# Optimization experiments

Hardware: AMD Instinct MI355X
Metric: run time of the kernel (lower is better)

The kernel has to match this reference:

```python
import jax, jax.numpy as jnp
import numpy as np
import math

B, S, E, D = 8, 2048, 1024, 1024  # batch, seq, emb_dim, encoder_emb_dim
LN_EPS = 1e-5
CLAMP = 1.0e9

def setup_inputs() -> dict:
    key = jax.random.key(0)
    ks = jax.random.split(key, 6)
    s = 1.0 / math.sqrt(E)
    return {
        "x": jax.random.normal(ks[0], (B, S, E), dtype=jnp.float32),
        "ln_w": jnp.ones((E,), jnp.float32),
        "ln_b": jnp.zeros((E,), jnp.float32),
        "wq": jax.random.normal(ks[1], (E, D), jnp.float32) * s,
        "bq": jnp.zeros((D,), jnp.float32),
        "wk": jax.random.normal(ks[2], (E, D), jnp.float32) * s,
        "bk": jnp.zeros((D,), jnp.float32),
        "wv": jax.random.normal(ks[3], (E, D), jnp.float32) * s,
        "bv": jnp.zeros((D,), jnp.float32),
        "w0": jax.random.normal(ks[4], (D, E), jnp.float32) * (1.0 / math.sqrt(D)),
        "b0": jnp.zeros((E,), jnp.float32),
    }

def reference(x, ln_w, ln_b, wq, bq, wk, bk, wv, bv, w0, b0):
    # LayerNorm over last dim (torch default eps=1e-5)
    mu = jnp.mean(x, axis=-1, keepdims=True)
    var = jnp.mean(jnp.square(x - mu), axis=-1, keepdims=True)
    xn = (x - mu) * jax.lax.rsqrt(var + LN_EPS) * ln_w + ln_b

    q = xn @ wq + bq  # [B,S,D]
    k = xn @ wk + bk
    v = xn @ wv + bv

    scale = math.sqrt(D) + 1e-9
    scores = jnp.einsum("bsd,btd->bst", q, k) / scale
    scores = jnp.clip(scores, -CLAMP, CLAMP)

    # masking=True, self_attending=True: mask = tril(ones, diagonal=-1)
    # i.e. positions t < s get -inf; diagonal stays unmasked (no NaN rows).
    mask = jnp.tril(jnp.ones((S, S), dtype=bool), k=-1)
    scores = jnp.where(mask, -jnp.inf, scores)

    a = jax.nn.softmax(scores, axis=-1)
    h = jnp.einsum("bst,btd->bsd", a, v)
    return h @ w0 + b0
```

## Files before the change

kernel.cpp:

```cpp
#include <hip/hip_runtime.h>
#include <cmath>

using u16 = unsigned short;
using u32 = unsigned int;
using bf16x8 = __attribute__((ext_vector_type(8))) __bf16;
using f32x4  = __attribute__((ext_vector_type(4))) float;

__device__ inline u16 f2bf(float f) {
  u32 u = __float_as_uint(f);
  u32 r = (u + 0x7fffu + ((u >> 16) & 1u)) >> 16;
  return (u16)r;
}
__device__ inline float bf2f(u16 v) { return __uint_as_float(((u32)v) << 16); }

__global__ __launch_bounds__(256) void prep1(
    const float* __restrict__ x, const float* __restrict__ lnw,
    const float* __restrict__ lnb, const float* __restrict__ wq,
    const float* __restrict__ wk, const float* __restrict__ wv,
    const float* __restrict__ w0, const float* __restrict__ bq,
    const float* __restrict__ bk, const float* __restrict__ bv,
    u16* __restrict__ xn, u16* __restrict__ w0t, u16* __restrict__ wqb,
    u16* __restrict__ wkb, u16* __restrict__ wvb, float* __restrict__ uvec,
    float* __restrict__ vvec, float* __restrict__ wb, float* __restrict__ sb) {
  int b = blockIdx.x;
  int tid = threadIdx.x;
  __shared__ float red[4];
  __shared__ float red2[4];
  int lane = tid & 63, wave = tid >> 6;
  if (b < 16384) {
    const float4* xr = (const float4*)(x + (size_t)b * 1024);
    float4 v = xr[tid];
    float s  = v.x + v.y + v.z + v.w;
    float ss = v.x * v.x + v.y * v.y + v.z * v.z + v.w * v.w;
#pragma unroll
    for (int o = 32; o >= 1; o >>= 1) {
      s  += __shfl_xor(s, o, 64);
      ss += __shfl_xor(ss, o, 64);
    }
    if (lane == 0) { red[wave] = s; red2[wave] = ss; }
    __syncthreads();
    s  = red[0] + red[1] + red[2] + red[3];
    ss = red2[0] + red2[1] + red2[2] + red2[3];
    float mean = s * (1.0f / 1024.0f);
    float var  = ss * (1.0f / 1024.0f) - mean * mean;
    float rstd = rsqrtf(var + 1e-5f);
    int c = tid * 4;
    ushort4 ov;
    ov.x = f2bf((v.x - mean) * rstd * lnw[c + 0] + lnb[c + 0]);
    ov.y = f2bf((v.y - mean) * rstd * lnw[c + 1] + lnb[c + 1]);
    ov.z = f2bf((v.z - mean) * rstd * lnw[c + 2] + lnb[c + 2]);
    ov.w = f2bf((v.w - mean) * rstd * lnw[c + 3] + lnb[c + 3]);
    ((ushort4*)(xn + (size_t)b * 1024))[tid] = ov;
  } else if (b < 17408) {
    int b2 = b - 16384;
    int c0 = (b2 & 31) * 32, r0 = (b2 >> 5) * 32;
    int tx = tid & 31, ty = tid >> 5;
    __shared__ float tile[32][33];
#pragma unroll
    for (int i = 0; i < 32; i += 8)
      tile[ty + i][tx] = w0[(size_t)(r0 + ty + i) * 1024 + c0 + tx];
    __syncthreads();
#pragma unroll
    for (int i = 0; i < 32; i += 8)
      w0t[(size_t)(c0 + ty + i) * 1024 + r0 + tx] = f2bf(tile[tx][ty + i]);
  } else if (b < 18944) {
    int b3 = b - 17408;
    int mat = b3 / 512, blk = b3 % 512;
    const float* src = (mat == 0) ? wq : (mat == 1) ? wk : wv;
    u16* dst = (mat == 0) ? wqb : (mat == 1) ? wkb : wvb;
    size_t base = (size_t)blk * 2048 + (size_t)tid * 8;
#pragma unroll
    for (int i = 0; i < 8; ++i) dst[base + i] = f2bf(src[base + i]);
  } else if (b < 22016) {
    int b4 = b - 18944;
    int which = b4 >> 10, idx = b4 & 1023;
    float p = 0.f;
    if (which == 0) {
      const float* r = wq + (size_t)idx * 1024;
      for (int e = tid * 4; e < (tid + 1) * 4; ++e) p += r[e] * bk[e];
    } else if (which == 1) {
      const float* r = wk + (size_t)idx * 1024;
      for (int e = tid * 4; e < (tid + 1) * 4; ++e) p += r[e] * bq[e];
    } else {
      for (int d = tid * 4; d < (tid + 1) * 4; ++d)
        p += bv[d] * w0[(size_t)d * 1024 + idx];
    }
#pragma unroll
    for (int o = 32; o >= 1; o >>= 1) p += __shfl_xor(p, o, 64);
    if (lane == 0) red[wave] = p;
    __syncthreads();
    if (tid == 0) {
      float t = red[0] + red[1] + red[2] + red[3];
      if (which == 0) uvec[idx] = t;
      else if (which == 1) vvec[idx] = t;
      else wb[idx] = t;
    }
  } else {
    float p = 0.f;
    for (int e = tid * 4; e < (tid + 1) * 4; ++e) p += bq[e] * bk[e];
#pragma unroll
    for (int o = 32; o >= 1; o >>= 1) p += __shfl_xor(p, o, 64);
    if (lane == 0) red[wave] = p;
    __syncthreads();
    if (tid == 0) sb[0] = red[0] + red[1] + red[2] + red[3];
  }
}

template <int OUTF32, int MODE>
__global__ __launch_bounds__(512, 2) void gemm256(
    const u16* __restrict__ A, const u16* __restrict__ B, void* __restrict__ Cv,
    const float* __restrict__ bias, int K, int lda, int ldb, int ldc,
    float scale, long long sA, long long sB, long long sC) {
  int gx = gridDim.x;
  int wg = blockIdx.y * gx + blockIdx.x;
  {
    int nwg = gx * gridDim.y;
    if ((nwg & 7) == 0) {
      int q = nwg >> 3;
      wg = (wg & 7) * q + (wg >> 3);
    }
  }
  const int ti = wg / gx, tj = wg % gx, bz = blockIdx.z;
  if (MODE == 1 && tj < ti) return;

  const u16* Ab = A + (size_t)bz * (size_t)sA;
  const u16* Bb = B + (size_t)bz * (size_t)sB;

  __shared__ u16 As[2][256 * 64];
  __shared__ u16 Bs[2][256 * 64];

  const int tid = threadIdx.x;
  const int wave = tid >> 6, lane = tid & 63;
  const int wr = wave >> 2, wc = wave & 3;
  const int fr = lane & 15;
  const int kb16 = (lane >> 4) * 16;
  const int swz = (fr & 7) << 4;
  const int cs0 = kb16 ^ swz;
  const int cs1 = (64 + kb16) ^ swz;
  const int aRowOff = (wr * 128 + fr) * 128;
  const int bRowOff = (wc * 64 + fr) * 128;

  size_t gAo[2][2], gBo[2][2];
  u32 ldsA[2][2], ldsB[2][2];
#pragma unroll
  for (int h = 0; h < 2; ++h) {
#pragma unroll
    for (int l = 0; l < 2; ++l) {
      int i = l * 512 + tid;
      int rih = i >> 3, ch8 = i & 7;
      int rA = (rih & 63) + ((rih >> 6) << 7) + h * 64;
      int cbA = (ch8 << 4) ^ ((rA & 7) << 4);
      gAo[h][l] = (size_t)rA * lda + (cbA >> 1);
      ldsA[h][l] = (u32)(rA * 8 + ch8) * 16;
      int rB = (rih & 31) + ((rih >> 5) << 6) + h * 32;
      int cbB = (ch8 << 4) ^ ((rB & 7) << 4);
      gBo[h][l] = (size_t)rB * ldb + (cbB >> 1);
      ldsB[h][l] = (u32)(rB * 8 + ch8) * 16;
    }
  }
  const size_t aBase = (size_t)(ti * 256) * lda;
  const size_t bBase = (size_t)(tj * 256) * ldb;

  const int k0 = (MODE == 2) ? ti * 256 : 0;
  const int niter = (K - k0) / 128;

  f32x4 acc[8][4] = {};
  bf16x8 aF[4][2], bF[4][2];

#define GLL(gaddr, laddr)                                        \
  __builtin_amdgcn_global_load_lds(                              \
      (const __attribute__((address_space(1))) void*)(gaddr),    \
      (__attribute__((address_space(3))) void*)(laddr), 16, 0, 0)

#define STAGE_A(buf, h, t)                                                     \
  do {                                                                         \
    const size_t _kt = aBase + (size_t)(k0 + (t) * 64);                        \
    GLL(Ab + _kt + gAo[h][0], (char*)&As[buf][0] + ldsA[h][0]);                \
    GLL(Ab + _kt + gAo[h][1], (char*)&As[buf][0] + ldsA[h][1]);                \
  } while (0)
#define STAGE_B(buf, h, t)                                                     \
  do {                                                                         \
    const size_t _kt = bBase + (size_t)(k0 + (t) * 64);                        \
    GLL(Bb + _kt + gBo[h][0], (char*)&Bs[buf][0] + ldsB[h][0]);                \
    GLL(Bb + _kt + gBo[h][1], (char*)&Bs[buf][0] + ldsB[h][1]);                \
  } while (0)

#define DS_A(buf, qm)                                                \
  do {                                                               \
    const char* _pa = (const char*)&As[buf][0] + aRowOff + (qm)*8192;\
    _Pragma("unroll") for (int mm = 0; mm < 4; ++mm) {               \
      aF[mm][0] = *(const bf16x8*)(_pa + mm * 2048 + cs0);           \
      aF[mm][1] = *(const bf16x8*)(_pa + mm * 2048 + cs1);           \
    }                                                                \
  } while (0)
#define DS_B(buf, nh)                                                \
  do {                                                               \
    const char* _pb = (const char*)&Bs[buf][0] + bRowOff;            \
    _Pragma("unroll") for (int nn = 0; nn < 2; ++nn) {               \
      bF[(nh)*2 + nn][0] = *(const bf16x8*)(_pb + ((nh)*2 + nn) * 2048 + cs0); \
      bF[(nh)*2 + nn][1] = *(const bf16x8*)(_pb + ((nh)*2 + nn) * 2048 + cs1); \
    }                                                                \
  } while (0)

#define MMA(qm, nh)                                                          \
  do {                                                                       \
    _Pragma("unroll") for (int mm = 0; mm < 4; ++mm)                         \
    _Pragma("unroll") for (int nn = 0; nn < 2; ++nn) {                       \
      f32x4 _c = acc[(qm)*4 + mm][(nh)*2 + nn];                              \
      _c = __builtin_amdgcn_mfma_f32_16x16x32_bf16(aF[mm][0], bF[(nh)*2+nn][0], _c, 0, 0, 0); \
      _c = __builtin_amdgcn_mfma_f32_16x16x32_bf16(aF[mm][1], bF[(nh)*2+nn][1], _c, 0, 0, 0); \
      acc[(qm)*4 + mm][(nh)*2 + nn] = _c;                                    \
    }                                                                        \
  } while (0)

#define BAR __builtin_amdgcn_s_barrier()
#define LGKM0 asm volatile("s_waitcnt lgkmcnt(0)" ::: "memory")
#define VM6 asm volatile("s_waitcnt vmcnt(6)" ::: "memory")
#define VM0 asm volatile("s_waitcnt vmcnt(0)" ::: "memory")
#define PRIO1 __builtin_amdgcn_s_setprio(1)
#define PRIO0 __builtin_amdgcn_s_setprio(0)

  STAGE_B(0, 0, 0); STAGE_B(0, 1, 0); STAGE_A(0, 0, 0); STAGE_A(0, 1, 0);
  STAGE_B(1, 0, 1); STAGE_B(1, 1, 1); STAGE_A(1, 0, 1);
  VM6; BAR;

  for (int it = 0; it < niter; ++it) {
    const bool last = (it == niter - 1);
    const int t1g = 2 * it + 1, t2g = 2 * it + 2, t3g = 2 * it + 3;

    DS_A(0, 0); DS_B(0, 0);
    STAGE_A(1, 1, t1g);
    BAR; LGKM0; PRIO1; MMA(0, 0); PRIO0; BAR;
    DS_B(0, 1);
    if (!last) STAGE_B(0, 0, t2g);
    BAR; LGKM0; PRIO1; MMA(0, 1); PRIO0; BAR;
    DS_A(0, 1);
    if (!last) STAGE_B(0, 1, t2g);
    BAR; LGKM0; PRIO1; MMA(1, 0); PRIO0; BAR;
    if (!last) STAGE_A(0, 0, t2g);
    BAR; PRIO1; MMA(1, 1); PRIO0;
    if (last) { VM0; } else { VM6; }
    BAR;
    DS_A(1, 0); DS_B(1, 0);
    if (!last) STAGE_A(0, 1, t2g);
    BAR; LGKM0; PRIO1; MMA(0, 0); PRIO0; BAR;
    DS_B(1, 1);
    if (!last) STAGE_B(1, 0, t3g);
    BAR; LGKM0; PRIO1; MMA(0, 1); PRIO0; BAR;
    DS_A(1, 1);
    if (!last) STAGE_B(1, 1, t3g);
    BAR; LGKM0; PRIO1; MMA(1, 0); PRIO0; BAR;
    if (!last) STAGE_A(1, 0, t3g);
    BAR; PRIO1; MMA(1, 1); PRIO0;
    if (!last) VM6;
    BAR;
  }

  const int orow0 = ti * 256 + wr * 128 + ((lane >> 4) << 2);
  const int ocol0 = tj * 256 + wc * 64 + fr;
#pragma unroll
  for (int m = 0; m < 8; ++m) {
#pragma unroll
    for (int n = 0; n < 4; ++n) {
      const int col = ocol0 + n * 16;
      const float bv = bias ? bias[col] : 0.0f;
#pragma unroll
      for (int j = 0; j < 4; ++j) {
        const int row = orow0 + m * 16 + j;
        const float v = acc[m][n][j] * scale + bv;
        const size_t idx = (size_t)bz * (size_t)sC + (size_t)row * ldc + col;
        if (OUTF32) ((float*)Cv)[idx] = v;
        else        ((u16*)Cv)[idx]   = f2bf(v);
      }
    }
  }
#undef GLL
#undef STAGE_A
#undef STAGE_B
#undef DS_A
#undef DS_B
#undef MMA
#undef BAR
#undef LGKM0
#undef VM6
#undef VM0
#undef PRIO1
#undef PRIO0
}

template <int BM, int EPI, int LDA, int LDB, int LDC, int KK, int K0CT>
__device__ __forceinline__ void gemm_body(
    const u16* __restrict__ Ab, const u16* __restrict__ Bb,
    void* __restrict__ Cp, const float* __restrict__ bias,
    const float* __restrict__ rbias, int rk0, float scale, size_t cbase,
    int ti, int tj, u16* __restrict__ AsP, u16* __restrict__ BsP,
    float* __restrict__ sumP, int dco,
    const float* __restrict__ ruP, const float* __restrict__ rvP) {
  constexpr int WM = BM / 2;
  constexpr int MH = BM / 64;
  constexpr int FM = 2 * MH;
  constexpr int HR = BM / 4;
  constexpr int LA = BM / 128;

  const int k0 = (K0CT >= 0) ? K0CT : rk0;

  const int tid = threadIdx.x;
  const int wave = tid >> 6, lane = tid & 63;
  const int wr = wave >> 2, wc = wave & 3;
  const int fr = lane & 15;
  const int kb16 = (lane >> 4) * 16;
  const int swz = (fr & 7) << 4;
  const int cs0 = kb16 ^ swz;
  const int cs1 = (64 + kb16) ^ swz;
  const int aRowOff = (wr * WM + fr) * 128;
  const int bRowOff = (wc * 64 + fr) * 128;

  __shared__ float invLds[(EPI == 2) ? BM : 1];
  if constexpr (EPI == 2) {
    if (tid < BM) {
      int s = ti * BM + tid;
      float a = 0.f;
      for (int q2 = s >> 8; q2 < 8; ++q2) a += sumP[q2 * 2048 + s];
      invLds[tid] = 1.0f / a;
    }
  }

  size_t gAo[2][LA], gBo[2][2];
  u32 ldsA[2][LA], ldsB[2][2];
#pragma unroll
  for (int h = 0; h < 2; ++h) {
#pragma unroll
    for (int l = 0; l < LA; ++l) {
      int i = l * 512 + tid;
      int rih = i >> 3, ch8 = i & 7;
      int rA = (rih % HR) + (rih / HR) * WM + h * HR;
      int cbA = (ch8 << 4) ^ ((rA & 7) << 4);
      gAo[h][l] = (size_t)rA * LDA + (cbA >> 1);
      ldsA[h][l] = (u32)(rA * 8 + ch8) * 16;
    }
#pragma unroll
    for (int l = 0; l < 2; ++l) {
      int i = l * 512 + tid;
      int rih = i >> 3, ch8 = i & 7;
      int rB = (rih & 31) + ((rih >> 5) << 6) + h * 32;
      int cbB = (ch8 << 4) ^ ((rB & 7) << 4);
      gBo[h][l] = (size_t)rB * LDB + (cbB >> 1);
      ldsB[h][l] = (u32)(rB * 8 + ch8) * 16;
    }
  }
  const size_t aBase = (size_t)(ti * BM) * LDA;
  const size_t bBase = (size_t)(tj * 256) * LDB;
  const int niter = (KK - k0) / 128;

  f32x4 acc[FM][4] = {};
  bf16x8 aF[MH][2], bF[4][2];

#define GLL(gaddr, laddr)                                        \
  __builtin_amdgcn_global_load_lds(                              \
      (const __attribute__((address_space(1))) void*)(gaddr),    \
      (__attribute__((address_space(3))) void*)(laddr), 16, 0, 0)

#define STAGE_A(buf, h, t)                                                   \
  do {                                                                       \
    const size_t _kt = aBase + (size_t)(k0 + (t) * 64);                      \
    _Pragma("unroll") for (int _l = 0; _l < LA; ++_l)                        \
        GLL(Ab + _kt + gAo[h][_l],                                           \
            (char*)(AsP + (buf) * (BM * 64)) + ldsA[h][_l]);                 \
  } while (0)
#define STAGE_B(buf, h, t)                                                   \
  do {                                                                       \
    const size_t _kt = bBase + (size_t)(k0 + (t) * 64);                      \
    _Pragma("unroll") for (int _l = 0; _l < 2; ++_l)                         \
        GLL(Bb + _kt + gBo[h][_l],                                           \
            (char*)(BsP + (buf) * (256 * 64)) + ldsB[h][_l]);                \
  } while (0)

#define DS_A(buf, qm)                                                        \
  do {                                                                       \
    const char* _pa =                                                        \
        (const char*)(AsP + (buf) * (BM * 64)) + aRowOff + (qm) * (MH * 2048); \
    _Pragma("unroll") for (int mm = 0; mm < MH; ++mm) {                      \
      aF[mm][0] = *(const bf16x8*)(_pa + mm * 2048 + cs0);                   \
      aF[mm][1] = *(const bf16x8*)(_pa + mm * 2048 + cs1);                   \
    }                                                                        \
  } while (0)
#define DS_B(buf, nh)                                                        \
  do {                                                                       \
    const char* _pb = (const char*)(BsP + (buf) * (256 * 64)) + bRowOff;     \
    _Pragma("unroll") for (int nn = 0; nn < 2; ++nn) {                       \
      bF[(nh)*2 + nn][0] = *(const bf16x8*)(_pb + ((nh)*2 + nn) * 2048 + cs0); \
      bF[(nh)*2 + nn][1] = *(const bf16x8*)(_pb + ((nh)*2 + nn) * 2048 + cs1); \
    }                                                                        \
  } while (0)

#define MMA(qm, nh)                                                          \
  do {                                                                       \
    _Pragma("unroll") for (int mm = 0; mm < MH; ++mm)                        \
    _Pragma("unroll") for (int nn = 0; nn < 2; ++nn) {                       \
      f32x4 _c = acc[(qm)*MH + mm][(nh)*2 + nn];                             \
      _c = __builtin_amdgcn_mfma_f32_16x16x32_bf16(aF[mm][0], bF[(nh)*2+nn][0], _c, 0, 0, 0); \
      _c = __builtin_amdgcn_mfma_f32_16x16x32_bf16(aF[mm][1], bF[(nh)*2+nn][1], _c, 0, 0, 0); \
      acc[(qm)*MH + mm][(nh)*2 + nn] = _c;                                   \
    }                                                                        \
  } while (0)

#define BAR __builtin_amdgcn_s_barrier()
#define LGKM0 asm volatile("s_waitcnt lgkmcnt(0)" ::: "memory")
#define VMN                                                                  \
  do {                                                                       \
    if constexpr (BM == 256)                                                 \
      asm volatile("s_waitcnt vmcnt(6)" ::: "memory");                       \
    else                                                                     \
      asm volatile("s_waitcnt vmcnt(5)" ::: "memory");                       \
  } while (0)
#define VM0 asm volatile("s_waitcnt vmcnt(0)" ::: "memory")
#define PRIO1 __builtin_amdgcn_s_setprio(1)
#define PRIO0 __builtin_amdgcn_s_setprio(0)

  STAGE_B(0, 0, 0); STAGE_B(0, 1, 0); STAGE_A(0, 0, 0); STAGE_A(0, 1, 0);
  STAGE_B(1, 0, 1); STAGE_B(1, 1, 1); STAGE_A(1, 0, 1);
  VMN; BAR;

#pragma unroll 1
  for (int it = 0; it < niter; ++it) {
    const bool last = (it == niter - 1);
    const int t1g = 2 * it + 1, t2g = 2 * it + 2, t3g = 2 * it + 3;

    DS_A(0, 0); DS_B(0, 0);
    STAGE_A(1, 1, t1g);
    BAR; LGKM0; PRIO1; MMA(0, 0); PRIO0; BAR;
    DS_B(0, 1);
    if (!last) STAGE_B(0, 0, t2g);
    BAR; LGKM0; PRIO1; MMA(0, 1); PRIO0; BAR;
    DS_A(0, 1);
    if (!last) STAGE_B(0, 1, t2g);
    BAR; LGKM0; PRIO1; MMA(1, 0); PRIO0; BAR;
    if (!last) STAGE_A(0, 0, t2g);
    BAR; PRIO1; MMA(1, 1); PRIO0;
    if (last) { VM0; } else { VMN; }
    BAR;
    DS_A(1, 0); DS_B(1, 0);
    if (!last) STAGE_A(0, 1, t2g);
    BAR; LGKM0; PRIO1; MMA(0, 0); PRIO0; BAR;
    DS_B(1, 1);
    if (!last) STAGE_B(1, 0, t3g);
    BAR; LGKM0; PRIO1; MMA(0, 1); PRIO0; BAR;
    DS_A(1, 1);
    if (!last) STAGE_B(1, 1, t3g);
    BAR; LGKM0; PRIO1; MMA(1, 0); PRIO0; BAR;
    if (!last) STAGE_A(1, 0, t3g);
    BAR; PRIO1; MMA(1, 1); PRIO0;
    if (!last) VMN;
    BAR;
  }

  const int orowL = wr * WM + ((lane >> 4) << 2);
  const int orow0 = ti * BM + orowL;
  const int ocol0 = tj * 256 + wc * 64 + fr;

  if constexpr (EPI == 1) {
    float* slds = (float*)AsP;
#pragma unroll
    for (int m = 0; m < FM; ++m) {
#pragma unroll
      for (int j = 0; j < 4; ++j) {
        const int rl = orowL + m * 16 + j;
        const int row = ti * BM + rl;
        const float ru = ruP[row];
        float rsum = 0.f;
#pragma unroll
        for (int n = 0; n < 4; ++n) {
          const int cl = wc * 64 + fr + n * 16;
          const int col = tj * 256 + cl;
          float v = (acc[m][n][j] + ru + rvP[col]) * scale;
          v = fminf(fmaxf(v, -1.0e9f), 1.0e9f);
          v = fminf(v, 60.0f);
          float e = __expf(v - 5.0f);
          if (cl < rl + dco) e = 0.f;
          rsum += e;
          ((u16*)Cp)[cbase + (size_t)row * LDC + col] = f2bf(e);
        }
        rsum += __shfl_xor(rsum, 1, 64);
        rsum += __shfl_xor(rsum, 2, 64);
        rsum += __shfl_xor(rsum, 4, 64);
        rsum += __shfl_xor(rsum, 8, 64);
        if (fr == 0) slds[rl * 4 + wc] = rsum;
      }
    }
    __syncthreads();
    if (tid < BM) {
      float t = slds[tid * 4 + 0] + slds[tid * 4 + 1] +
                slds[tid * 4 + 2] + slds[tid * 4 + 3];
      sumP[ti * BM + tid] = t;
    }
  } else {
#pragma unroll
    for (int m = 0; m < FM; ++m) {
#pragma unroll
      for (int j = 0; j < 4; ++j) {
        const int row = orow0 + m * 16 + j;
        float mul = (EPI == 2) ? invLds[orowL + m * 16 + j] : 1.0f;
        float rb = (EPI == 0 && rbias) ? rbias[row] : 0.0f;
#pragma unroll
        for (int n = 0; n < 4; ++n) {
          const int col = ocol0 + n * 16;
          const float bv = bias ? bias[col] : 0.0f;
          const size_t idx = cbase + (size_t)row * LDC + col;
          if constexpr (EPI == 2) {
            ((float*)Cp)[idx] = acc[m][n][j] * mul + bv;
          } else {
            ((u16*)Cp)[idx] = f2bf(acc[m][n][j] + bv + rb);
          }
        }
      }
    }
  }
#undef GLL
#undef STAGE_A
#undef STAGE_B
#undef DS_A
#undef DS_B
#undef MMA
#undef BAR
#undef LGKM0
#undef VMN
#undef VM0
#undef PRIO1
#undef PRIO0
}

__global__ __launch_bounds__(512, 2) void prep2(
    const u16* __restrict__ wqb, const u16* __restrict__ wkb,
    const u16* __restrict__ wvb, const u16* __restrict__ w0t,
    const u16* __restrict__ xn, const float* __restrict__ uvec,
    const float* __restrict__ vvec, const float* __restrict__ sb,
    u16* __restrict__ Gt, u16* __restrict__ Uw,
    float* __restrict__ ru, float* __restrict__ rv) {
  __shared__ u16 As[2][128 * 64];
  __shared__ u16 Bs[2][256 * 64];
  int b = blockIdx.x;
  if (b < 32) {
    int ti = b & 7, tj = b >> 3;
    gemm_body<128, 0, 1024, 1024, 1024, 1024, 0>(
        wkb, wqb, Gt, nullptr, nullptr, 0, 1.0f, 0, ti, tj,
        &As[0][0], &Bs[0][0], nullptr, 0, nullptr, nullptr);
  } else if (b < 64) {
    int b2 = b - 32;
    int ti = b2 & 7, tj = b2 >> 3;
    gemm_body<128, 0, 1024, 1024, 1024, 1024, 0>(
        w0t, wvb, Uw, nullptr, nullptr, 0, 1.0f, 0, ti, tj,
        &As[0][0], &Bs[0][0], nullptr, 0, nullptr, nullptr);
  } else {
    int r = b - 64;
    int tid = threadIdx.x;
    const u16* row = xn + (size_t)r * 1024;
    float pu = 0.f, pv = 0.f;
    int c = tid * 2;
    float x0 = bf2f(row[c]), x1 = bf2f(row[c + 1]);
    pu = x0 * uvec[c] + x1 * uvec[c + 1];
    pv = x0 * vvec[c] + x1 * vvec[c + 1];
#pragma unroll
    for (int o = 32; o >= 1; o >>= 1) {
      pu += __shfl_xor(pu, o, 64);
      pv += __shfl_xor(pv, o, 64);
    }
    __shared__ float rdu[8], rdv[8];
    int lane = tid & 63, wave = tid >> 6;
    if (lane == 0) { rdu[wave] = pu; rdv[wave] = pv; }
    __syncthreads();
    if (tid == 0) {
      float su = 0.f, sv = 0.f;
#pragma unroll
      for (int w = 0; w < 8; ++w) { su += rdu[w]; sv += rdv[w]; }
      ru[r] = su + sb[0];
      rv[r] = sv;
    }
  }
}

__global__ __launch_bounds__(512, 2) void wt_kernel(
    const u16* __restrict__ Uw, const u16* __restrict__ xn,
    u16* __restrict__ Wt, const float* __restrict__ wb) {
  __shared__ u16 As[2][128 * 64];
  __shared__ u16 Bs[2][256 * 64];
  int x = blockIdx.x;
  int bz = x & 7, o = x >> 3;
  int ti = o & 7, tj = o >> 3;
  gemm_body<128, 0, 1024, 1024, 2048, 1024, 0>(
      Uw, xn + (size_t)bz * 2048 * 1024, Wt, nullptr, wb, 0, 1.0f,
      (size_t)bz * 1024 * 2048, ti, tj, &As[0][0], &Bs[0][0],
      nullptr, 0, nullptr, nullptr);
}

__global__ __launch_bounds__(512, 2) void qk_kernel(
    const u16* __restrict__ xnG, const u16* __restrict__ xn,
    u16* __restrict__ sc, float* __restrict__ sumP,
    const float* __restrict__ ru, const float* __restrict__ rv,
    int b0, int nb, float qk_scale) {
  __shared__ u16 As[2][128 * 64];
  __shared__ u16 Bs[2][256 * 64];
  int x = blockIdx.x;
  int bzl = x % nb, t72 = x / nb;
  int bz = b0 + bzl;
  int tq = 0, rem = t72;
  for (;;) { int L = 8 - (tq >> 1); if (rem < L) break; rem -= L; ++tq; }
  int tj = (tq >> 1) + rem;
  int dco = tq * 128 - tj * 256;
  gemm_body<128, 1, 1024, 1024, 2048, 1024, 0>(
      xnG + (size_t)bz * 2048 * 1024, xn + (size_t)bz * 2048 * 1024, sc,
      nullptr, nullptr, 0, qk_scale, (size_t)bzl * 2048 * 2048, tq, tj,
      &As[0][0], &Bs[0][0], sumP + ((size_t)bz * 8 + tj) * 2048, dco,
      ru + (size_t)bz * 2048, rv + (size_t)bz * 2048);
}

__global__ __launch_bounds__(512, 2) void gemm_pv(
    const u16* __restrict__ sc, const u16* __restrict__ Wt,
    float* __restrict__ out, const float* __restrict__ b0v,
    float* __restrict__ sumP, int nb, int bA) {
  __shared__ u16 As[2][128 * 64];
  __shared__ u16 Bs[2][256 * 64];
  int x = blockIdx.x;
  int bzl = x % nb;
  int rem = x / nb;
  int ti = rem >> 2, tj = rem & 3;
  int bz = bA + bzl;
  gemm_body<128, 2, 2048, 2048, 1024, 2048, -1>(
      sc + (size_t)bzl * 2048 * 2048, Wt + (size_t)bz * 1024 * 2048, out, b0v,
      nullptr, ti * 128, 1.0f, (size_t)bz * 2048 * 1024, ti, tj,
      &As[0][0], &Bs[0][0], sumP + (size_t)bz * 8 * 2048, 0,
      nullptr, nullptr);
}

extern "C" void kernel_launch(void* const* d_in, const int* in_sizes, int n_in,
                              void* d_out, int out_size, void* d_ws, size_t ws_size,
                              hipStream_t stream) {
  (void)in_sizes; (void)n_in; (void)out_size;
  const float* x   = (const float*)d_in[0];
  const float* lnw = (const float*)d_in[1];
  const float* lnb = (const float*)d_in[2];
  const float* wq  = (const float*)d_in[3];
  const float* bq  = (const float*)d_in[4];
  const float* wk  = (const float*)d_in[5];
  const float* bk  = (const float*)d_in[6];
  const float* wv  = (const float*)d_in[7];
  const float* bv  = (const float*)d_in[8];
  const float* w0  = (const float*)d_in[9];
  const float* b0  = (const float*)d_in[10];
  float* out = (float*)d_out;

  const size_t ROWS = 16384;
  char* ws = (char*)d_ws;
  size_t off = 0;
  auto alloc = [&](size_t bytes) -> void* {
    void* p = ws + off;
    off += (bytes + 255) & ~(size_t)255;
    return p;
  };
  u16*   xn   = (u16*)alloc(ROWS * 1024 * 2);
  u16*   w0t  = (u16*)alloc((size_t)1024 * 1024 * 2);
  u16*   wqb  = (u16*)alloc((size_t)1024 * 1024 * 2);
  u16*   wkb  = (u16*)alloc((size_t)1024 * 1024 * 2);
  u16*   wvb  = (u16*)alloc((size_t)1024 * 1024 * 2);
  u16*   Gt   = (u16*)alloc((size_t)1024 * 1024 * 2);
  u16*   Uw   = (u16*)alloc((size_t)1024 * 1024 * 2);
  float* uvec = (float*)alloc(1024 * 4);
  float* vvec = (float*)alloc(1024 * 4);
  float* wb   = (float*)alloc(1024 * 4);
  float* sb   = (float*)alloc(256);
  float* ru   = (float*)alloc(ROWS * 4);
  float* rv   = (float*)alloc(ROWS * 4);
  float* sumP = (float*)alloc((size_t)8 * 8 * 2048 * 4);
  u16*   xnG  = (u16*)alloc(ROWS * 1024 * 2);
  u16*   Wt   = (u16*)alloc(ROWS * 1024 * 2);

  const size_t CHUNK1 = (size_t)2048 * 2048 * 2;
  size_t avail = (ws_size > off) ? ws_size - off : 0;
  int NBCH = (int)(avail / CHUNK1);
  if (NBCH > 8) NBCH = 8;
  if (NBCH < 1) NBCH = 1;
  u16* sc = (u16*)(ws + off);

  prep1<<<dim3(22017), dim3(256), 0, stream>>>(
      x, lnw, lnb, wq, wk, wv, w0, bq, bk, bv,
      xn, w0t, wqb, wkb, wvb, uvec, vvec, wb, sb);
  prep2<<<dim3(64 + 16384), dim3(512), 0, stream>>>(
      wqb, wkb, wvb, w0t, xn, uvec, vvec, sb, Gt, Uw, ru, rv);
  gemm256<0, 0><<<dim3(4, 64, 1), dim3(512), 0, stream>>>(
      xn, Gt, xnG, nullptr, 1024, 1024, 1024, 1024, 1.0f, 0, 0, 0);
  wt_kernel<<<dim3(512), dim3(512), 0, stream>>>(Uw, xn, Wt, wb);

  float qk_scale = (float)(1.0 / (std::sqrt(1024.0) + 1e-9));

  for (int bA = 0; bA < 8; bA += NBCH) {
    int nb = 8 - bA;
    if (nb > NBCH) nb = NBCH;
    qk_kernel<<<dim3(nb * 72), dim3(512), 0, stream>>>(
        xnG, xn, sc, sumP, ru, rv, bA, nb, qk_scale);
    gemm_pv<<<dim3(64 * nb), dim3(512), 0, stream>>>(
        sc, Wt, out, b0, sumP, nb, bA);
  }
}
```

Before: 320.4 us.

## Fuse Wt GEMM into QK kernel with 256-row tiles and split row-dot kernel

Merges the separate Wt GEMM launch into the QK score kernel as extra blocks on the first chunk. The QK tiles grow from 128 to 256 rows, halving the tile count and improving reuse, though this doubles the A shared-memory buffer and may cut occupancy. The per-row u/v dot products move out of prep2 into a dedicated kernel with one wave per row, replacing 16384 blocks that used a block-wide reduction. Together these aim to cut launch count, tail effects and reduction overhead, at the risk of load imbalance between heterogeneous block types.

```diff
diff --git a/kernel.cpp b/kernel.cpp
--- a/kernel.cpp
+++ b/kernel.cpp
@@ -104,6 +104,29 @@
     __syncthreads();
     if (tid == 0) sb[0] = red[0] + red[1] + red[2] + red[3];
   }
+}
+
+__global__ __launch_bounds__(512) void ruv_kernel(
+    const u16* __restrict__ xn, const float* __restrict__ uvec,
+    const float* __restrict__ vvec, const float* __restrict__ sb,
+    float* __restrict__ ru, float* __restrict__ rv) {
+  int wv = threadIdx.x >> 6, lane = threadIdx.x & 63;
+  int r = blockIdx.x * 8 + wv;
+  const u16* row = xn + (size_t)r * 1024;
+  int c0 = lane * 16;
+  float pu = 0.f, pv = 0.f;
+#pragma unroll
+  for (int i = 0; i < 16; ++i) {
+    float xv = bf2f(row[c0 + i]);
+    pu += xv * uvec[c0 + i];
+    pv += xv * vvec[c0 + i];
+  }
+#pragma unroll
+  for (int o = 32; o >= 1; o >>= 1) {
+    pu += __shfl_xor(pu, o, 64);
+    pv += __shfl_xor(pv, o, 64);
+  }
+  if (lane == 0) { ru[r] = pu + sb[0]; rv[r] = pv; }
 }
 
 template <int OUTF32, int MODE>
@@ -532,10 +555,7 @@
 __global__ __launch_bounds__(512, 2) void prep2(
     const u16* __restrict__ wqb, const u16* __restrict__ wkb,
     const u16* __restrict__ wvb, const u16* __restrict__ w0t,
-    const u16* __restrict__ xn, const float* __restrict__ uvec,
-    const float* __restrict__ vvec, const float* __restrict__ sb,
-    u16* __restrict__ Gt, u16* __restrict__ Uw,
-    float* __restrict__ ru, float* __restrict__ rv) {
+    u16* __restrict__ Gt, u16* __restrict__ Uw) {
   __shared__ u16 As[2][128 * 64];
   __shared__ u16 Bs[2][256 * 64];
   int b = blockIdx.x;
@@ -544,73 +564,46 @@
     gemm_body<128, 0, 1024, 1024, 1024, 1024, 0>(
         wkb, wqb, Gt, nullptr, nullptr, 0, 1.0f, 0, ti, tj,
         &As[0][0], &Bs[0][0], nullptr, 0, nullptr, nullptr);
-  } else if (b < 64) {
+  } else {
     int b2 = b - 32;
     int ti = b2 & 7, tj = b2 >> 3;
     gemm_body<128, 0, 1024, 1024, 1024, 1024, 0>(
         w0t, wvb, Uw, nullptr, nullptr, 0, 1.0f, 0, ti, tj,
         &As[0][0], &Bs[0][0], nullptr, 0, nullptr, nullptr);
+  }
+}
+
+__global__ __launch_bounds__(512, 2) void gemm_qkwt(
+    const u16* __restrict__ xnG, const u16* __restrict__ xn,
+    const u16* __restrict__ Uw, u16* __restrict__ Wt, u16* __restrict__ sc,
+    float* __restrict__ sumP, const float* __restrict__ ru,
+    const float* __restrict__ rv, const float* __restrict__ wb,
+    int qkBlocks, int b0, int nb, float qk_scale) {
+  __shared__ u16 As[2][256 * 64];
+  __shared__ u16 Bs[2][256 * 64];
+  const long long sXN = 2048LL * 1024, sWt = 1024LL * 2048, sS = 2048LL * 2048;
+  int x = blockIdx.x;
+  if (x < qkBlocks) {
+    int bzl = x % nb, t36 = x / nb;
+    int bz = b0 + bzl;
+    int tq = 0, rem = t36;
+    for (;;) { int L = 8 - tq; if (rem < L) break; rem -= L; ++tq; }
+    int tj = tq + rem;
+    gemm_body<256, 1, 1024, 1024, 2048, 1024, 0>(
+        xnG + (size_t)bz * sXN, xn + (size_t)bz * sXN, sc, nullptr, nullptr,
+        0, qk_scale, (size_t)bzl * sS, tq, tj, &As[0][0], &Bs[0][0],
+        sumP + ((size_t)bz * 8 + tj) * 2048, (tq - tj) * 256,
+        ru + (size_t)bz * 2048, rv + (size_t)bz * 2048);
   } else {
-    int r = b - 64;
-    int tid = threadIdx.x;
-    const u16* row = xn + (size_t)r * 1024;
-    float pu = 0.f, pv = 0.f;
-    int c = tid * 2;
-    float x0 = bf2f(row[c]), x1 = bf2f(row[c + 1]);
-    pu = x0 * uvec[c] + x1 * uvec[c + 1];
-    pv = x0 * vvec[c] + x1 * vvec[c + 1];
-#pragma unroll
-    for (int o = 32; o >= 1; o >>= 1) {
-      pu += __shfl_xor(pu, o, 64);
-      pv += __shfl_xor(pv, o, 64);
-    }
-    __shared__ float rdu[8], rdv[8];
-    int lane = tid & 63, wave = tid >> 6;
-    if (lane == 0) { rdu[wave] = pu; rdv[wave] = pv; }
-    __syncthreads();
-    if (tid == 0) {
-      float su = 0.f, sv = 0.f;
-#pragma unroll
-      for (int w = 0; w < 8; ++w) { su += rdu[w]; sv += rdv[w]; }
-      ru[r] = su + sb[0];
-      rv[r] = sv;
-    }
-  }
-}
-
-__global__ __launch_bounds__(512, 2) void wt_kernel(
-    const u16* __restrict__ Uw, const u16* __restrict__ xn,
-    u16* __restrict__ Wt, const float* __restrict__ wb) {
-  __shared__ u16 As[2][128 * 64];
-  __shared__ u16 Bs[2][256 * 64];
-  int x = blockIdx.x;
-  int bz = x & 7, o = x >> 3;
-  int ti = o & 7, tj = o >> 3;
-  gemm_body<128, 0, 1024, 1024, 2048, 1024, 0>(
-      Uw, xn + (size_t)bz * 2048 * 1024, Wt, nullptr, wb, 0, 1.0f,
-      (size_t)bz * 1024 * 2048, ti, tj, &As[0][0], &Bs[0][0],
-      nullptr, 0, nullptr, nullptr);
-}
-
-__global__ __launch_bounds__(512, 2) void qk_kernel(
-    const u16* __restrict__ xnG, const u16* __restrict__ xn,
-    u16* __restrict__ sc, float* __restrict__ sumP,
-    const float* __restrict__ ru, const float* __restrict__ rv,
-    int b0, int nb, float qk_scale) {
-  __shared__ u16 As[2][128 * 64];
-  __shared__ u16 Bs[2][256 * 64];
-  int x = blockIdx.x;
-  int bzl = x % nb, t72 = x / nb;
-  int bz = b0 + bzl;
-  int tq = 0, rem = t72;
-  for (;;) { int L = 8 - (tq >> 1); if (rem < L) break; rem -= L; ++tq; }
-  int tj = (tq >> 1) + rem;
-  int dco = tq * 128 - tj * 256;
-  gemm_body<128, 1, 1024, 1024, 2048, 1024, 0>(
-      xnG + (size_t)bz * 2048 * 1024, xn + (size_t)bz * 2048 * 1024, sc,
-      nullptr, nullptr, 0, qk_scale, (size_t)bzl * 2048 * 2048, tq, tj,
-      &As[0][0], &Bs[0][0], sumP + ((size_t)bz * 8 + tj) * 2048, dco,
-      ru + (size_t)bz * 2048, rv + (size_t)bz * 2048);
+    int x2 = x - qkBlocks;
+    int bz = x2 & 7;
+    int o = x2 >> 3;
+    int ti = o & 7, tj = o >> 3;
+    gemm_body<128, 0, 1024, 1024, 2048, 1024, 0>(
+        Uw, xn + (size_t)bz * sXN, Wt, nullptr, wb, 0, 1.0f,
+        (size_t)bz * sWt, ti, tj, &As[0][0], &Bs[0][0],
+        nullptr, 0, nullptr, nullptr);
+  }
 }
 
 __global__ __launch_bounds__(512, 2) void gemm_pv(
@@ -683,19 +676,20 @@
   prep1<<<dim3(22017), dim3(256), 0, stream>>>(
       x, lnw, lnb, wq, wk, wv, w0, bq, bk, bv,
       xn, w0t, wqb, wkb, wvb, uvec, vvec, wb, sb);
-  prep2<<<dim3(64 + 16384), dim3(512), 0, stream>>>(
-      wqb, wkb, wvb, w0t, xn, uvec, vvec, sb, Gt, Uw, ru, rv);
+  prep2<<<dim3(64), dim3(512), 0, stream>>>(wqb, wkb, wvb, w0t, Gt, Uw);
+  ruv_kernel<<<dim3(2048), dim3(512), 0, stream>>>(xn, uvec, vvec, sb, ru, rv);
   gemm256<0, 0><<<dim3(4, 64, 1), dim3(512), 0, stream>>>(
       xn, Gt, xnG, nullptr, 1024, 1024, 1024, 1024, 1.0f, 0, 0, 0);
-  wt_kernel<<<dim3(512), dim3(512), 0, stream>>>(Uw, xn, Wt, wb);
 
   float qk_scale = (float)(1.0 / (std::sqrt(1024.0) + 1e-9));
 
   for (int bA = 0; bA < 8; bA += NBCH) {
     int nb = 8 - bA;
     if (nb > NBCH) nb = NBCH;
-    qk_kernel<<<dim3(nb * 72), dim3(512), 0, stream>>>(
-        xnG, xn, sc, sumP, ru, rv, bA, nb, qk_scale);
+    int qkB = nb * 36;
+    int wtB = (bA == 0) ? 512 : 0;
+    gemm_qkwt<<<dim3(qkB + wtB), dim3(512), 0, stream>>>(
+        xnG, xn, Uw, Wt, sc, sumP, ru, rv, wb, qkB, bA, nb, qk_scale);
     gemm_pv<<<dim3(64 * nb), dim3(512), 0, stream>>>(
         sc, Wt, out, b0, sumP, nb, bA);
   }
```

New measurement: 265.0 us, median of 2. 17.3% less time.
